# Optimization experiments

Measured on AMD Instinct MI355X. Metric: run time of the kernel, lower is better.

Reference implementation:

```python
import jax, jax.numpy as jnp
import numpy as np

N = 100000      # nodes
E = 1600000     # edges
IN_C = 64       # in_channels
HID = 128       # hidden_channels
K = 2           # Chebyshev order
EPS = 1e-5      # BatchNorm eps
SLOPE = 0.01    # LeakyReLU negative slope


def _glorot(key, shape, fan_in):
    lim = 1.0 / np.sqrt(fan_in)
    return jax.random.uniform(key, shape, jnp.float32, -lim, lim)


def setup_inputs() -> dict:
    key = jax.random.key(0)
    ks = jax.random.split(key, 12)
    x = jax.random.normal(ks[0], (N, IN_C), jnp.float32)
    edge_index = jax.random.randint(ks[1], (2, E), 0, N, dtype=jnp.int32)
    # ChebConv weights: one [Cin, Cout] matrix per Chebyshev order, plus bias.
    W1 = _glorot(ks[2], (K, IN_C, HID), IN_C)
    b1 = _glorot(ks[3], (HID,), IN_C)
    W2 = _glorot(ks[4], (K, HID, HID // 2), HID)
    b2 = _glorot(ks[5], (HID // 2,), HID)
    W3 = _glorot(ks[6], (K, HID // 2, IN_C), HID // 2)
    b3 = _glorot(ks[7], (IN_C,), HID // 2)
    # BatchNorm affine params
    gamma1 = jnp.ones((HID,), jnp.float32)
    beta1 = jnp.zeros((HID,), jnp.float32)
    gamma2 = jnp.ones((HID // 2,), jnp.float32)
    beta2 = jnp.zeros((HID // 2,), jnp.float32)
    return {"x": x, "edge_index": edge_index, "W1": W1, "b1": b1,
            "W2": W2, "b2": b2, "W3": W3, "b3": b3,
            "gamma1": gamma1, "beta1": beta1, "gamma2": gamma2, "beta2": beta2}


def reference(x, edge_index, W1, b1, W2, b2, W3, b3, gamma1, beta1, gamma2, beta2):
    row, col = edge_index[0], edge_index[1]
    # Scaled Laplacian with lambda_max=2 (PyG default): L_hat = -D^{-1/2} A D^{-1/2}
    deg = jax.ops.segment_sum(jnp.ones(row.shape, x.dtype), row, num_segments=N)
    dinv = jnp.where(deg > 0, jax.lax.rsqrt(jnp.where(deg > 0, deg, 1.0)), 0.0)
    ew = -dinv[row] * dinv[col]                     # [E] edge weights of L_hat

    def prop(h):  # y = L_hat @ h ; gather from source, scatter to target
        return jax.ops.segment_sum(ew[:, None] * h[row], col, num_segments=N)

    def cheb_conv(h, W, b):  # K=2: Tx0 = h, Tx1 = L_hat @ h
        return h @ W[0] + prop(h) @ W[1] + b

    def batchnorm(h, g, b):  # training-mode BN over node dim, biased variance
        m = h.mean(axis=0)
        v = jnp.mean(jnp.square(h - m), axis=0)
        return g * (h - m) * jax.lax.rsqrt(v + EPS) + b

    def lrelu(h):
        return jnp.where(h >= 0, h, SLOPE * h)

    h = lrelu(batchnorm(cheb_conv(x, W1, b1), gamma1, beta1))
    h = lrelu(batchnorm(cheb_conv(h, W2, b2), gamma2, beta2))
    return cheb_conv(h, W3, b3)
```

## Files before the change

kernel.cpp:

```cpp
#include <hip/hip_runtime.h>

#define NN 100000
#define NE 1600000
constexpr float BN_EPS = 1e-5f;
constexpr float LRELU_SLOPE = 0.01f;
constexpr int SC_NB = (NN + 255) / 256;
constexpr int RSH = 13;
constexpr int RB = 1 << RSH;
constexpr int NR = (NN + RB - 1) / RB;
constexpr int SB = 8;
constexpr int CAP = 163840;
constexpr int PBLK = 400;
constexpr int PCHUNK = NE / PBLK;

__global__ __launch_bounds__(256) void k_part(const int* __restrict__ row,
                                              const int* __restrict__ col,
                                              int* __restrict__ colCnt,
                                              int* __restrict__ rowCnt,
                                              int* __restrict__ colbuf,
                                              unsigned short* __restrict__ rowbuf) {
  __shared__ int cntc[NR], cntr[NR];
  const int tid = threadIdx.x;
  const int e0 = blockIdx.x * PCHUNK;
  if (tid < NR) { cntc[tid] = 0; cntr[tid] = 0; }
  __syncthreads();
  for (int i = tid; i < PCHUNK; i += 256) {
    atomicAdd(&cntc[col[e0 + i] >> RSH], 1);
    atomicAdd(&cntr[row[e0 + i] >> RSH], 1);
  }
  __syncthreads();
  if (tid < NR) {
    cntc[tid] = atomicAdd(&colCnt[tid], cntc[tid]);
  } else if (tid >= 64 && tid < 64 + NR) {
    const int b = tid - 64;
    cntr[b] = atomicAdd(&rowCnt[b], cntr[b]);
  }
  __syncthreads();
  for (int i = tid; i < PCHUNK; i += 256) {
    const int r = row[e0 + i];
    const int c = col[e0 + i];
    const int bc = c >> RSH;
    const int pc = atomicAdd(&cntc[bc], 1);
    colbuf[(size_t)bc * CAP + pc] = (r << RSH) | (c & (RB - 1));
    const int br = r >> RSH;
    const int pr = atomicAdd(&cntr[br], 1);
    rowbuf[(size_t)br * CAP + pr] = (unsigned short)(r & (RB - 1));
  }
}

__global__ __launch_bounds__(1024) void k_hist2(const int* __restrict__ colbuf,
                                                const unsigned short* __restrict__ rowbuf,
                                                const int* __restrict__ colCnt,
                                                const int* __restrict__ rowCnt,
                                                int* __restrict__ PDc,
                                                int* __restrict__ PDd) {
  __shared__ int h[RB];
  const int tid = threadIdx.x;
  const int b = blockIdx.x, s = blockIdx.y, z = blockIdx.z;
  for (int i = tid; i < RB; i += 1024) h[i] = 0;
  __syncthreads();
  const int len = z ? rowCnt[b] : colCnt[b];
  const int sl = (len + SB - 1) / SB;
  const int st = s * sl;
  const int en = min(st + sl, len);
  if (z == 0) {
    const int* cb = colbuf + (size_t)b * CAP;
    for (int i = st + tid; i < en; i += 1024)
      atomicAdd(&h[cb[i] & (RB - 1)], 1);
  } else {
    const unsigned short* rb = rowbuf + (size_t)b * CAP;
    for (int i = st + tid; i < en; i += 1024)
      atomicAdd(&h[rb[i]], 1);
  }
  __syncthreads();
  int* pd = (z ? PDd : PDc) + ((size_t)b * SB + s) * RB;
  for (int i = tid; i < RB; i += 1024) pd[i] = h[i];
}

__global__ __launch_bounds__(256) void k_csrmid2(const int* __restrict__ PDc,
                                                 const int* __restrict__ PDd,
                                                 int* __restrict__ Bpart,
                                                 int* __restrict__ cnt,
                                                 float* __restrict__ dinv) {
  const int n = blockIdx.x * 256 + threadIdx.x;
  if (n >= NN) return;
  const int b = n >> RSH, o = n & (RB - 1);
  int run = 0, dsum = 0;
#pragma unroll
  for (int s = 0; s < SB; s++) {
    Bpart[(size_t)s * NN + n] = run;
    run += PDc[((size_t)b * SB + s) * RB + o];
    dsum += PDd[((size_t)b * SB + s) * RB + o];
  }
  cnt[n] = run;
  dinv[n] = dsum > 0 ? rsqrtf((float)dsum) : 0.0f;
}

__global__ __launch_bounds__(256) void k_scan_a(const int* __restrict__ cnt,
                                                int* __restrict__ bsum) {
  __shared__ int sh[256];
  const int tid = threadIdx.x;
  const int i = blockIdx.x * 256 + tid;
  sh[tid] = (i < NN) ? cnt[i] : 0;
  __syncthreads();
  for (int st = 128; st > 0; st >>= 1) {
    if (tid < st) sh[tid] += sh[tid + st];
    __syncthreads();
  }
  if (tid == 0) bsum[blockIdx.x] = sh[0];
}

__global__ __launch_bounds__(512) void k_scan_b(const int* __restrict__ bsum,
                                                int* __restrict__ boff) {
  __shared__ int sh[512];
  const int tid = threadIdx.x;
  const int v = (tid < SC_NB) ? bsum[tid] : 0;
  sh[tid] = v;
  __syncthreads();
  for (int off = 1; off < 512; off <<= 1) {
    int t = (tid >= off) ? sh[tid - off] : 0;
    __syncthreads();
    sh[tid] += t;
    __syncthreads();
  }
  if (tid < SC_NB) boff[tid] = sh[tid] - v;
}

__global__ __launch_bounds__(256) void k_scan_c(const int* __restrict__ cnt,
                                                const int* __restrict__ boff,
                                                int* __restrict__ ptr) {
  __shared__ int sh[256];
  const int tid = threadIdx.x;
  const int i = blockIdx.x * 256 + tid;
  const int v = (i < NN) ? cnt[i] : 0;
  sh[tid] = v;
  __syncthreads();
  for (int off = 1; off < 256; off <<= 1) {
    int t = (tid >= off) ? sh[tid - off] : 0;
    __syncthreads();
    sh[tid] += t;
    __syncthreads();
  }
  const int excl = sh[tid] - v + boff[blockIdx.x];
  if (i < NN) {
    ptr[i] = excl;
    if (i == NN - 1) ptr[NN] = excl + v;
  }
}

__global__ __launch_bounds__(1024) void k_fill4(const int* __restrict__ colbuf,
                                                const int* __restrict__ colCnt,
                                                const int* __restrict__ ptr,
                                                const int* __restrict__ Bpart,
                                                int* __restrict__ eb) {
  __shared__ int cur[RB];
  const int tid = threadIdx.x;
  const int b = blockIdx.x, s = blockIdx.y;
  const int base = b << RSH;
  const int nmax = min(RB, NN - base);
  const int* bp = Bpart + (size_t)s * NN + base;
  for (int i = tid; i < nmax; i += 1024) cur[i] = ptr[base + i] + bp[i];
  __syncthreads();
  const int len = colCnt[b];
  const int sl = (len + SB - 1) / SB;
  const int st = s * sl;
  const int en = min(st + sl, len);
  const int* cb = colbuf + (size_t)b * CAP;
  for (int i = st + tid; i < en; i += 1024) {
    const int rec = cb[i];
    const int pos = atomicAdd(&cur[rec & (RB - 1)], 1);
    eb[pos] = rec >> RSH;
  }
}

__global__ __launch_bounds__(256) void k_scale(const float* __restrict__ x,
                                               const float* __restrict__ dinv,
                                               float* __restrict__ xs) {
  const size_t i = (size_t)blockIdx.x * 256 + threadIdx.x;
  const int n = (int)(i >> 4);
  float4 v = reinterpret_cast<const float4*>(x)[i];
  const float d = dinv[n];
  v.x *= d; v.y *= d; v.z *= d; v.w *= d;
  reinterpret_cast<float4*>(xs)[i] = v;
}

template <bool ADD>
__global__ __launch_bounds__(256) void k_prop64(const float* __restrict__ p,
                                                const int* __restrict__ eb,
                                                const int* __restrict__ ptr,
                                                const float* __restrict__ g,
                                                const float* __restrict__ dinv,
                                                float* __restrict__ out) {
  const int node = blockIdx.x * 16 + (threadIdx.x >> 4);
  const int lane = threadIdx.x & 15;
  if (node >= NN) return;
  const int b = ptr[node], e = ptr[node + 1];
  float4 a0 = make_float4(0.f, 0.f, 0.f, 0.f);
  float4 a1 = make_float4(0.f, 0.f, 0.f, 0.f);
  float4 a2 = make_float4(0.f, 0.f, 0.f, 0.f);
  float4 a3 = make_float4(0.f, 0.f, 0.f, 0.f);
  const float4* hp = reinterpret_cast<const float4*>(p) + lane;
  int j = b;
  for (; j + 4 <= e; j += 4) {
    const int s0 = eb[j], s1 = eb[j + 1], s2 = eb[j + 2], s3 = eb[j + 3];
    const float4 h0 = hp[(size_t)s0 * 16];
    const float4 h1 = hp[(size_t)s1 * 16];
    const float4 h2 = hp[(size_t)s2 * 16];
    const float4 h3 = hp[(size_t)s3 * 16];
    a0.x += h0.x; a0.y += h0.y; a0.z += h0.z; a0.w += h0.w;
    a1.x += h1.x; a1.y += h1.y; a1.z += h1.z; a1.w += h1.w;
    a2.x += h2.x; a2.y += h2.y; a2.z += h2.z; a2.w += h2.w;
    a3.x += h3.x; a3.y += h3.y; a3.z += h3.z; a3.w += h3.w;
  }
  for (; j + 2 <= e; j += 2) {
    const int s0 = eb[j], s1 = eb[j + 1];
    const float4 h0 = hp[(size_t)s0 * 16];
    const float4 h1 = hp[(size_t)s1 * 16];
    a0.x += h0.x; a0.y += h0.y; a0.z += h0.z; a0.w += h0.w;
    a1.x += h1.x; a1.y += h1.y; a1.z += h1.z; a1.w += h1.w;
  }
  if (j < e) {
    const float4 h0 = hp[(size_t)eb[j] * 16];
    a0.x += h0.x; a0.y += h0.y; a0.z += h0.z; a0.w += h0.w;
  }
  a0.x += a1.x + a2.x + a3.x;
  a0.y += a1.y + a2.y + a3.y;
  a0.z += a1.z + a2.z + a3.z;
  a0.w += a1.w + a2.w + a3.w;
  if (ADD) {
    const float dn = dinv[node];
    const float4 gv = reinterpret_cast<const float4*>(g)[(size_t)node * 16 + lane];
    a0.x = gv.x - dn * a0.x;
    a0.y = gv.y - dn * a0.y;
    a0.z = gv.z - dn * a0.z;
    a0.w = gv.w - dn * a0.w;
  }
  reinterpret_cast<float4*>(out)[(size_t)node * 16 + lane] = a0;
}

__global__ __launch_bounds__(512) void k_conv1(const float* __restrict__ x,
                                               const float* __restrict__ y,
                                               const float* __restrict__ dinv,
                                               const float* __restrict__ W,
                                               const float* __restrict__ bias,
                                               float* __restrict__ out) {
  __shared__ float XA[128][65];
  __shared__ float XY[128][65];
  const int tid = threadIdx.x;
  const int lane = tid & 63;
  const int wv = __builtin_amdgcn_readfirstlane(tid >> 6);
  const int n0 = blockIdx.x * 128;
  for (int idx = tid; idx < 2048; idx += 512) {
    const int n = idx >> 4, k4 = idx & 15;
    int node = n0 + n;
    if (node >= NN) node = NN - 1;
    const float4 av = *reinterpret_cast<const float4*>(x + (size_t)node * 64 + k4 * 4);
    float4 yv = *reinterpret_cast<const float4*>(y + (size_t)node * 64 + k4 * 4);
    const float dn = -dinv[node];
    yv.x *= dn; yv.y *= dn; yv.z *= dn; yv.w *= dn;
    float* da = &XA[n][k4 * 4];
    da[0] = av.x; da[1] = av.y; da[2] = av.z; da[3] = av.w;
    float* dy = &XY[n][k4 * 4];
    dy[0] = yv.x; dy[1] = yv.y; dy[2] = yv.z; dy[3] = yv.w;
  }
  __syncthreads();
  const int cw0 = wv * 16;
  const float* __restrict__ W0 = W + cw0;
  const float* __restrict__ W1 = W + 64 * 128 + cw0;
  float acc0[16], acc1[16];
#pragma unroll
  for (int j = 0; j < 16; j++) { acc0[j] = 0.f; acc1[j] = 0.f; }
#pragma unroll 2
  for (int k = 0; k < 64; k++) {
    const float a0 = XA[lane][k];
    const float a1 = XA[lane + 64][k];
    const float b0 = XY[lane][k];
    const float b1 = XY[lane + 64][k];
#pragma unroll
    for (int j = 0; j < 16; j++) {
      const float w0 = W0[(size_t)k * 128 + j];
      const float w1 = W1[(size_t)k * 128 + j];
      acc0[j] += a0 * w0 + b0 * w1;
      acc1[j] += a1 * w0 + b1 * w1;
    }
  }
#pragma unroll
  for (int half = 0; half < 2; half++) {
    const int node = n0 + lane + half * 64;
    const float* acc = half ? acc1 : acc0;
    if (node < NN) {
#pragma unroll
      for (int j = 0; j < 16; j += 4) {
        float4 o = make_float4(acc[j] + bias[cw0 + j], acc[j + 1] + bias[cw0 + j + 1],
                               acc[j + 2] + bias[cw0 + j + 2], acc[j + 3] + bias[cw0 + j + 3]);
        *reinterpret_cast<float4*>(out + (size_t)node * 128 + cw0 + j) = o;
      }
    }
  }
}

template <int Cin>
__global__ __launch_bounds__(512) void k_gemm_dual(const float* __restrict__ h,
                                                   const float* __restrict__ W,
                                                   const float* __restrict__ bias,
                                                   const float* __restrict__ scale,
                                                   const float* __restrict__ shift,
                                                   const float* __restrict__ dinv,
                                                   float* __restrict__ g,
                                                   float* __restrict__ p) {
  __shared__ float XA[128][Cin + 1];
  const int tid = threadIdx.x;
  const int lane = tid & 63;
  const int wv = __builtin_amdgcn_readfirstlane(tid >> 6);
  const int n0 = blockIdx.x * 128;
  constexpr int C4 = Cin / 4;
  for (int idx = tid; idx < 128 * C4; idx += 512) {
    const int n = idx / C4, k4 = idx % C4;
    int node = n0 + n;
    if (node >= NN) node = NN - 1;
    float4 v = *reinterpret_cast<const float4*>(h + (size_t)node * Cin + k4 * 4);
    const float4 sc = *reinterpret_cast<const float4*>(scale + k4 * 4);
    const float4 sh = *reinterpret_cast<const float4*>(shift + k4 * 4);
    v.x = sc.x * v.x + sh.x; v.y = sc.y * v.y + sh.y;
    v.z = sc.z * v.z + sh.z; v.w = sc.w * v.w + sh.w;
    v.x = v.x >= 0.f ? v.x : LRELU_SLOPE * v.x;
    v.y = v.y >= 0.f ? v.y : LRELU_SLOPE * v.y;
    v.z = v.z >= 0.f ? v.z : LRELU_SLOPE * v.z;
    v.w = v.w >= 0.f ? v.w : LRELU_SLOPE * v.w;
    float* d = &XA[n][k4 * 4];
    d[0] = v.x; d[1] = v.y; d[2] = v.z; d[3] = v.w;
  }
  __syncthreads();
  const int cw0 = wv * 8;
  const float* __restrict__ Wa = W + cw0;
  const float* __restrict__ Wb = W + Cin * 64 + cw0;
  float ag0[8], ag1[8], ap0[8], ap1[8];
#pragma unroll
  for (int j = 0; j < 8; j++) { ag0[j] = 0.f; ag1[j] = 0.f; ap0[j] = 0.f; ap1[j] = 0.f; }
#pragma unroll 2
  for (int k = 0; k < Cin; k++) {
    const float a0 = XA[lane][k];
    const float a1 = XA[lane + 64][k];
#pragma unroll
    for (int j = 0; j < 8; j++) {
      const float wa = Wa[(size_t)k * 64 + j];
      const float wb = Wb[(size_t)k * 64 + j];
      ag0[j] += a0 * wa; ag1[j] += a1 * wa;
      ap0[j] += a0 * wb; ap1[j] += a1 * wb;
    }
  }
#pragma unroll
  for (int half = 0; half < 2; half++) {
    const int node = n0 + lane + half * 64;
    const float* ag = half ? ag1 : ag0;
    const float* ap = half ? ap1 : ap0;
    if (node < NN) {
      const float dn = dinv[node];
#pragma unroll
      for (int j = 0; j < 8; j += 4) {
        float4 og = make_float4(ag[j] + bias[cw0 + j], ag[j + 1] + bias[cw0 + j + 1],
                                ag[j + 2] + bias[cw0 + j + 2], ag[j + 3] + bias[cw0 + j + 3]);
        *reinterpret_cast<float4*>(g + (size_t)node * 64 + cw0 + j) = og;
        float4 op = make_float4(ap[j] * dn, ap[j + 1] * dn, ap[j + 2] * dn, ap[j + 3] * dn);
        *reinterpret_cast<float4*>(p + (size_t)node * 64 + cw0 + j) = op;
      }
    }
  }
}

template <int C>
__global__ __launch_bounds__(256) void k_bnstats(const float* __restrict__ h,
                                                 float* __restrict__ bnsum,
                                                 float* __restrict__ bnsq) {
  constexpr int RPB = 256 / C;
  constexpr int ROWS = 256;
  const int c = threadIdx.x % C;
  const int g = threadIdx.x / C;
  const int r0 = blockIdx.x * ROWS + g;
  const int rend = min(blockIdx.x * ROWS + ROWS, NN);
  float s = 0.f, sq = 0.f;
  for (int r = r0; r < rend; r += RPB) {
    float v = h[(size_t)r * C + c];
    s += v;
    sq += v * v;
  }
  __shared__ float ss[256], sg[256];
  ss[threadIdx.x] = s;
  sg[threadIdx.x] = sq;
  __syncthreads();
  for (int st = 128; st >= C; st >>= 1) {
    if (threadIdx.x < st) {
      ss[threadIdx.x] += ss[threadIdx.x + st];
      sg[threadIdx.x] += sg[threadIdx.x + st];
    }
    __syncthreads();
  }
  if (threadIdx.x < C) {
    atomicAdd(&bnsum[threadIdx.x], ss[threadIdx.x]);
    atomicAdd(&bnsq[threadIdx.x], sg[threadIdx.x]);
  }
}

template <int C>
__global__ void k_bnfin(const float* __restrict__ bnsum, const float* __restrict__ bnsq,
                        const float* __restrict__ gamma, const float* __restrict__ beta,
                        float* __restrict__ scale, float* __restrict__ shift) {
  int c = threadIdx.x;
  if (c < C) {
    float mean = bnsum[c] * (1.0f / NN);
    float var = bnsq[c] * (1.0f / NN) - mean * mean;
    float sc = gamma[c] * rsqrtf(var + BN_EPS);
    scale[c] = sc;
    shift[c] = beta[c] - mean * sc;
  }
}

extern "C" void kernel_launch(void* const* d_in, const int* in_sizes, int n_in,
                              void* d_out, int out_size, void* d_ws, size_t ws_size,
                              hipStream_t stream) {
  const float* x   = (const float*)d_in[0];
  const int*   ei  = (const int*)d_in[1];
  const int*   row = ei;
  const int*   col = ei + NE;
  const float* W1  = (const float*)d_in[2];
  const float* b1  = (const float*)d_in[3];
  const float* W2  = (const float*)d_in[4];
  const float* b2  = (const float*)d_in[5];
  const float* W3  = (const float*)d_in[6];
  const float* b3  = (const float*)d_in[7];
  const float* g1  = (const float*)d_in[8];
  const float* be1 = (const float*)d_in[9];
  const float* g2w = (const float*)d_in[10];
  const float* be2 = (const float*)d_in[11];
  float* out = (float*)d_out;

  char* ws = (char*)d_ws;
  size_t off = 0;
  auto alloc = [&](size_t bytes) -> void* {
    void* p = ws + off;
    off = (off + bytes + 255) & ~(size_t)255;
    return p;
  };

  float* bnsum1 = (float*)alloc(128 * 4);
  float* bnsq1  = (float*)alloc(128 * 4);
  float* bnsum2 = (float*)alloc(64 * 4);
  float* bnsq2  = (float*)alloc(64 * 4);
  int*   colCnt = (int*)alloc(NR * 4);
  int*   rowCnt = (int*)alloc(NR * 4);
  const size_t zero_bytes = off;
  float* dinv   = (float*)alloc(NN * 4);
  int*   cnt    = (int*)alloc(NN * 4);
  int*   ptr    = (int*)alloc((NN + 1) * 4);
  int*   bsum   = (int*)alloc(SC_NB * 4);
  int*   boff   = (int*)alloc(SC_NB * 4);
  int*   eb     = (int*)alloc((size_t)NE * 4);
  float* scale1 = (float*)alloc(128 * 4);
  float* shift1 = (float*)alloc(128 * 4);
  float* scale2 = (float*)alloc(64 * 4);
  float* shift2 = (float*)alloc(64 * 4);
  float* bufA   = (float*)alloc((size_t)NN * 64 * 4);
  float* bufB   = (float*)alloc((size_t)NN * 128 * 4);
  float* bufC   = (float*)alloc((size_t)NN * 64 * 4);
  float* bufD   = (float*)alloc((size_t)NN * 64 * 4);

  int* colbuf = (int*)bufB;
  unsigned short* rowbuf = (unsigned short*)(colbuf + (size_t)NR * CAP);
  int* PDc    = (int*)bufC;
  int* PDd    = PDc + (size_t)NR * SB * RB;
  int* Bpart  = PDd + (size_t)NR * SB * RB;

  float* y1  = bufA;
  float* xs  = bufC;
  float* h1  = bufB;
  float* gg2 = bufA;
  float* p2  = bufC;
  float* h2  = bufD;
  float* gg3 = bufB;
  float* p3  = bufB + (size_t)NN * 64;

  hipMemsetAsync(d_ws, 0, zero_bytes, stream);

  k_part<<<PBLK, 256, 0, stream>>>(row, col, colCnt, rowCnt, colbuf, rowbuf);
  k_hist2<<<dim3(NR, SB, 2), 1024, 0, stream>>>(colbuf, rowbuf, colCnt, rowCnt, PDc, PDd);
  k_csrmid2<<<(NN + 255) / 256, 256, 0, stream>>>(PDc, PDd, Bpart, cnt, dinv);
  k_scan_a<<<SC_NB, 256, 0, stream>>>(cnt, bsum);
  k_scan_b<<<1, 512, 0, stream>>>(bsum, boff);
  k_scan_c<<<SC_NB, 256, 0, stream>>>(cnt, boff, ptr);
  k_fill4<<<dim3(NR, SB), 1024, 0, stream>>>(colbuf, colCnt, ptr, Bpart, eb);

  const int gemmGrid = (NN + 127) / 128;
  const int propGrid = (NN * 16 + 255) / 256;

  k_scale<<<NN * 16 / 256, 256, 0, stream>>>(x, dinv, xs);
  k_prop64<false><<<propGrid, 256, 0, stream>>>(xs, eb, ptr, nullptr, nullptr, y1);
  k_conv1<<<gemmGrid, 512, 0, stream>>>(x, y1, dinv, W1, b1, h1);
  k_bnstats<128><<<(NN + 255) / 256, 256, 0, stream>>>(h1, bnsum1, bnsq1);
  k_bnfin<128><<<1, 128, 0, stream>>>(bnsum1, bnsq1, g1, be1, scale1, shift1);

  k_gemm_dual<128><<<gemmGrid, 512, 0, stream>>>(h1, W2, b2, scale1, shift1, dinv, gg2, p2);
  k_prop64<true><<<propGrid, 256, 0, stream>>>(p2, eb, ptr, gg2, dinv, h2);
  k_bnstats<64><<<(NN + 255) / 256, 256, 0, stream>>>(h2, bnsum2, bnsq2);
  k_bnfin<64><<<1, 64, 0, stream>>>(bnsum2, bnsq2, g2w, be2, scale2, shift2);

  k_gemm_dual<64><<<gemmGrid, 512, 0, stream>>>(h2, W3, b3, scale2, shift2, dinv, gg3, p3);
  k_prop64<true><<<propGrid, 256, 0, stream>>>(p3, eb, ptr, gg3, dinv, out);
}
```

Measured before the change: 573.9 us.

## Fuse source scaling into first propagation and halve GEMM node tiles

Removes the separate k_scale pass by having the first propagation kernel multiply each gathered source row by dinv[src] on the fly, saving one full read/write of x. The conv1 and dual GEMM kernels now handle 64 nodes per block instead of 128, with padded shared rows and vectorised float2/float4 LDS reads and writes. This doubles the grid and lowers register pressure, but each weight load is reused across fewer nodes, and the fused propagation adds a scattered dinv load per edge.

```diff
diff --git a/kernel.cpp b/kernel.cpp
--- a/kernel.cpp
+++ b/kernel.cpp
@@ -173,18 +173,7 @@
   }
 }
 
-__global__ __launch_bounds__(256) void k_scale(const float* __restrict__ x,
-                                               const float* __restrict__ dinv,
-                                               float* __restrict__ xs) {
-  const size_t i = (size_t)blockIdx.x * 256 + threadIdx.x;
-  const int n = (int)(i >> 4);
-  float4 v = reinterpret_cast<const float4*>(x)[i];
-  const float d = dinv[n];
-  v.x *= d; v.y *= d; v.z *= d; v.w *= d;
-  reinterpret_cast<float4*>(xs)[i] = v;
-}
-
-template <bool ADD>
+template <bool SCALE, bool ADD>
 __global__ __launch_bounds__(256) void k_prop64(const float* __restrict__ p,
                                                 const int* __restrict__ eb,
                                                 const int* __restrict__ ptr,
@@ -203,25 +192,35 @@
   int j = b;
   for (; j + 4 <= e; j += 4) {
     const int s0 = eb[j], s1 = eb[j + 1], s2 = eb[j + 2], s3 = eb[j + 3];
+    const float w0 = SCALE ? dinv[s0] : 1.f;
+    const float w1 = SCALE ? dinv[s1] : 1.f;
+    const float w2 = SCALE ? dinv[s2] : 1.f;
+    const float w3 = SCALE ? dinv[s3] : 1.f;
     const float4 h0 = hp[(size_t)s0 * 16];
     const float4 h1 = hp[(size_t)s1 * 16];
     const float4 h2 = hp[(size_t)s2 * 16];
     const float4 h3 = hp[(size_t)s3 * 16];
-    a0.x += h0.x; a0.y += h0.y; a0.z += h0.z; a0.w += h0.w;
-    a1.x += h1.x; a1.y += h1.y; a1.z += h1.z; a1.w += h1.w;
-    a2.x += h2.x; a2.y += h2.y; a2.z += h2.z; a2.w += h2.w;
-    a3.x += h3.x; a3.y += h3.y; a3.z += h3.z; a3.w += h3.w;
-  }
-  for (; j + 2 <= e; j += 2) {
-    const int s0 = eb[j], s1 = eb[j + 1];
+    if (SCALE) {
+      a0.x += w0 * h0.x; a0.y += w0 * h0.y; a0.z += w0 * h0.z; a0.w += w0 * h0.w;
+      a1.x += w1 * h1.x; a1.y += w1 * h1.y; a1.z += w1 * h1.z; a1.w += w1 * h1.w;
+      a2.x += w2 * h2.x; a2.y += w2 * h2.y; a2.z += w2 * h2.z; a2.w += w2 * h2.w;
+      a3.x += w3 * h3.x; a3.y += w3 * h3.y; a3.z += w3 * h3.z; a3.w += w3 * h3.w;
+    } else {
+      a0.x += h0.x; a0.y += h0.y; a0.z += h0.z; a0.w += h0.w;
+      a1.x += h1.x; a1.y += h1.y; a1.z += h1.z; a1.w += h1.w;
+      a2.x += h2.x; a2.y += h2.y; a2.z += h2.z; a2.w += h2.w;
+      a3.x += h3.x; a3.y += h3.y; a3.z += h3.z; a3.w += h3.w;
+    }
+  }
+  for (; j < e; j++) {
+    const int s0 = eb[j];
+    const float w0 = SCALE ? dinv[s0] : 1.f;
     const float4 h0 = hp[(size_t)s0 * 16];
-    const float4 h1 = hp[(size_t)s1 * 16];
-    a0.x += h0.x; a0.y += h0.y; a0.z += h0.z; a0.w += h0.w;
-    a1.x += h1.x; a1.y += h1.y; a1.z += h1.z; a1.w += h1.w;
-  }
-  if (j < e) {
-    const float4 h0 = hp[(size_t)eb[j] * 16];
-    a0.x += h0.x; a0.y += h0.y; a0.z += h0.z; a0.w += h0.w;
+    if (SCALE) {
+      a0.x += w0 * h0.x; a0.y += w0 * h0.y; a0.z += w0 * h0.z; a0.w += w0 * h0.w;
+    } else {
+      a0.x += h0.x; a0.y += h0.y; a0.z += h0.z; a0.w += h0.w;
+    }
   }
   a0.x += a1.x + a2.x + a3.x;
   a0.y += a1.y + a2.y + a3.y;
@@ -244,13 +243,14 @@
                                                const float* __restrict__ W,
                                                const float* __restrict__ bias,
                                                float* __restrict__ out) {
-  __shared__ float XA[128][65];
-  __shared__ float XY[128][65];
+  constexpr int LDW = 68;
+  __shared__ float XA[64][LDW];
+  __shared__ float XY[64][LDW];
   const int tid = threadIdx.x;
   const int lane = tid & 63;
   const int wv = __builtin_amdgcn_readfirstlane(tid >> 6);
-  const int n0 = blockIdx.x * 128;
-  for (int idx = tid; idx < 2048; idx += 512) {
+  const int n0 = blockIdx.x * 64;
+  for (int idx = tid; idx < 1024; idx += 512) {
     const int n = idx >> 4, k4 = idx & 15;
     int node = n0 + n;
     if (node >= NN) node = NN - 1;
@@ -258,43 +258,35 @@
     float4 yv = *reinterpret_cast<const float4*>(y + (size_t)node * 64 + k4 * 4);
     const float dn = -dinv[node];
     yv.x *= dn; yv.y *= dn; yv.z *= dn; yv.w *= dn;
-    float* da = &XA[n][k4 * 4];
-    da[0] = av.x; da[1] = av.y; da[2] = av.z; da[3] = av.w;
-    float* dy = &XY[n][k4 * 4];
-    dy[0] = yv.x; dy[1] = yv.y; dy[2] = yv.z; dy[3] = yv.w;
+    *reinterpret_cast<float4*>(&XA[n][k4 * 4]) = av;
+    *reinterpret_cast<float4*>(&XY[n][k4 * 4]) = yv;
   }
   __syncthreads();
   const int cw0 = wv * 16;
   const float* __restrict__ W0 = W + cw0;
   const float* __restrict__ W1 = W + 64 * 128 + cw0;
-  float acc0[16], acc1[16];
-#pragma unroll
-  for (int j = 0; j < 16; j++) { acc0[j] = 0.f; acc1[j] = 0.f; }
+  float acc[16];
+#pragma unroll
+  for (int j = 0; j < 16; j++) acc[j] = 0.f;
 #pragma unroll 2
-  for (int k = 0; k < 64; k++) {
-    const float a0 = XA[lane][k];
-    const float a1 = XA[lane + 64][k];
-    const float b0 = XY[lane][k];
-    const float b1 = XY[lane + 64][k];
-#pragma unroll
-    for (int j = 0; j < 16; j++) {
-      const float w0 = W0[(size_t)k * 128 + j];
-      const float w1 = W1[(size_t)k * 128 + j];
-      acc0[j] += a0 * w0 + b0 * w1;
-      acc1[j] += a1 * w0 + b1 * w1;
-    }
-  }
-#pragma unroll
-  for (int half = 0; half < 2; half++) {
-    const int node = n0 + lane + half * 64;
-    const float* acc = half ? acc1 : acc0;
-    if (node < NN) {
-#pragma unroll
-      for (int j = 0; j < 16; j += 4) {
-        float4 o = make_float4(acc[j] + bias[cw0 + j], acc[j + 1] + bias[cw0 + j + 1],
-                               acc[j + 2] + bias[cw0 + j + 2], acc[j + 3] + bias[cw0 + j + 3]);
-        *reinterpret_cast<float4*>(out + (size_t)node * 128 + cw0 + j) = o;
-      }
+  for (int kc = 0; kc < 32; kc++) {
+    const float2 a2 = *reinterpret_cast<const float2*>(&XA[lane][kc * 2]);
+    const float2 y2 = *reinterpret_cast<const float2*>(&XY[lane][kc * 2]);
+    const int k0 = kc * 2;
+#pragma unroll
+    for (int j = 0; j < 16; j++)
+      acc[j] += a2.x * W0[(size_t)k0 * 128 + j] + y2.x * W1[(size_t)k0 * 128 + j];
+#pragma unroll
+    for (int j = 0; j < 16; j++)
+      acc[j] += a2.y * W0[(size_t)(k0 + 1) * 128 + j] + y2.y * W1[(size_t)(k0 + 1) * 128 + j];
+  }
+  const int node = n0 + lane;
+  if (node < NN) {
+#pragma unroll
+    for (int j = 0; j < 16; j += 4) {
+      float4 o = make_float4(acc[j] + bias[cw0 + j], acc[j + 1] + bias[cw0 + j + 1],
+                             acc[j + 2] + bias[cw0 + j + 2], acc[j + 3] + bias[cw0 + j + 3]);
+      *reinterpret_cast<float4*>(out + (size_t)node * 128 + cw0 + j) = o;
     }
   }
 }
@@ -308,13 +300,14 @@
                                                    const float* __restrict__ dinv,
                                                    float* __restrict__ g,
                                                    float* __restrict__ p) {
-  __shared__ float XA[128][Cin + 1];
+  constexpr int LDW = Cin + 4;
+  __shared__ float XA[64][LDW];
   const int tid = threadIdx.x;
   const int lane = tid & 63;
   const int wv = __builtin_amdgcn_readfirstlane(tid >> 6);
-  const int n0 = blockIdx.x * 128;
+  const int n0 = blockIdx.x * 64;
   constexpr int C4 = Cin / 4;
-  for (int idx = tid; idx < 128 * C4; idx += 512) {
+  for (int idx = tid; idx < 64 * C4; idx += 512) {
     const int n = idx / C4, k4 = idx % C4;
     int node = n0 + n;
     if (node >= NN) node = NN - 1;
@@ -327,43 +320,50 @@
     v.y = v.y >= 0.f ? v.y : LRELU_SLOPE * v.y;
     v.z = v.z >= 0.f ? v.z : LRELU_SLOPE * v.z;
     v.w = v.w >= 0.f ? v.w : LRELU_SLOPE * v.w;
-    float* d = &XA[n][k4 * 4];
-    d[0] = v.x; d[1] = v.y; d[2] = v.z; d[3] = v.w;
+    *reinterpret_cast<float4*>(&XA[n][k4 * 4]) = v;
   }
   __syncthreads();
   const int cw0 = wv * 8;
   const float* __restrict__ Wa = W + cw0;
   const float* __restrict__ Wb = W + Cin * 64 + cw0;
-  float ag0[8], ag1[8], ap0[8], ap1[8];
-#pragma unroll
-  for (int j = 0; j < 8; j++) { ag0[j] = 0.f; ag1[j] = 0.f; ap0[j] = 0.f; ap1[j] = 0.f; }
+  float ag[8], ap[8];
+#pragma unroll
+  for (int j = 0; j < 8; j++) { ag[j] = 0.f; ap[j] = 0.f; }
 #pragma unroll 2
-  for (int k = 0; k < Cin; k++) {
-    const float a0 = XA[lane][k];
-    const float a1 = XA[lane + 64][k];
+  for (int kc = 0; kc < C4; kc++) {
+    const float4 a4 = *reinterpret_cast<const float4*>(&XA[lane][kc * 4]);
+    const int k0 = kc * 4;
 #pragma unroll
     for (int j = 0; j < 8; j++) {
-      const float wa = Wa[(size_t)k * 64 + j];
-      const float wb = Wb[(size_t)k * 64 + j];
-      ag0[j] += a0 * wa; ag1[j] += a1 * wa;
-      ap0[j] += a0 * wb; ap1[j] += a1 * wb;
-    }
-  }
-#pragma unroll
-  for (int half = 0; half < 2; half++) {
-    const int node = n0 + lane + half * 64;
-    const float* ag = half ? ag1 : ag0;
-    const float* ap = half ? ap1 : ap0;
-    if (node < NN) {
-      const float dn = dinv[node];
-#pragma unroll
-      for (int j = 0; j < 8; j += 4) {
-        float4 og = make_float4(ag[j] + bias[cw0 + j], ag[j + 1] + bias[cw0 + j + 1],
-                                ag[j + 2] + bias[cw0 + j + 2], ag[j + 3] + bias[cw0 + j + 3]);
-        *reinterpret_cast<float4*>(g + (size_t)node * 64 + cw0 + j) = og;
-        float4 op = make_float4(ap[j] * dn, ap[j + 1] * dn, ap[j + 2] * dn, ap[j + 3] * dn);
-        *reinterpret_cast<float4*>(p + (size_t)node * 64 + cw0 + j) = op;
-      }
+      ag[j] += a4.x * Wa[(size_t)k0 * 64 + j];
+      ap[j] += a4.x * Wb[(size_t)k0 * 64 + j];
+    }
+#pragma unroll
+    for (int j = 0; j < 8; j++) {
+      ag[j] += a4.y * Wa[(size_t)(k0 + 1) * 64 + j];
+      ap[j] += a4.y * Wb[(size_t)(k0 + 1) * 64 + j];
+    }
+#pragma unroll
+    for (int j = 0; j < 8; j++) {
+      ag[j] += a4.z * Wa[(size_t)(k0 + 2) * 64 + j];
+      ap[j] += a4.z * Wb[(size_t)(k0 + 2) * 64 + j];
+    }
+#pragma unroll
+    for (int j = 0; j < 8; j++) {
+      ag[j] += a4.w * Wa[(size_t)(k0 + 3) * 64 + j];
+      ap[j] += a4.w * Wb[(size_t)(k0 + 3) * 64 + j];
+    }
+  }
+  const int node = n0 + lane;
+  if (node < NN) {
+    const float dn = dinv[node];
+#pragma unroll
+    for (int j = 0; j < 8; j += 4) {
+      float4 og = make_float4(ag[j] + bias[cw0 + j], ag[j + 1] + bias[cw0 + j + 1],
+                              ag[j + 2] + bias[cw0 + j + 2], ag[j + 3] + bias[cw0 + j + 3]);
+      *reinterpret_cast<float4*>(g + (size_t)node * 64 + cw0 + j) = og;
+      float4 op = make_float4(ap[j] * dn, ap[j + 1] * dn, ap[j + 2] * dn, ap[j + 3] * dn);
+      *reinterpret_cast<float4*>(p + (size_t)node * 64 + cw0 + j) = op;
     }
   }
 }
@@ -471,7 +471,6 @@
   int* Bpart  = PDd + (size_t)NR * SB * RB;
 
   float* y1  = bufA;
-  float* xs  = bufC;
   float* h1  = bufB;
   float* gg2 = bufA;
   float* p2  = bufC;
@@ -489,20 +488,19 @@
   k_scan_c<<<SC_NB, 256, 0, stream>>>(cnt, boff, ptr);
   k_fill4<<<dim3(NR, SB), 1024, 0, stream>>>(colbuf, colCnt, ptr, Bpart, eb);
 
-  const int gemmGrid = (NN + 127) / 128;
+  const int gemmGrid = (NN + 63) / 64;
   const int propGrid = (NN * 16 + 255) / 256;
 
-  k_scale<<<NN * 16 / 256, 256, 0, stream>>>(x, dinv, xs);
-  k_prop64<false><<<propGrid, 256, 0, stream>>>(xs, eb, ptr, nullptr, nullptr, y1);
+  k_prop64<true, false><<<propGrid, 256, 0, stream>>>(x, eb, ptr, nullptr, dinv, y1);
   k_conv1<<<gemmGrid, 512, 0, stream>>>(x, y1, dinv, W1, b1, h1);
   k_bnstats<128><<<(NN + 255) / 256, 256, 0, stream>>>(h1, bnsum1, bnsq1);
   k_bnfin<128><<<1, 128, 0, stream>>>(bnsum1, bnsq1, g1, be1, scale1, shift1);
 
   k_gemm_dual<128><<<gemmGrid, 512, 0, stream>>>(h1, W2, b2, scale1, shift1, dinv, gg2, p2);
-  k_prop64<true><<<propGrid, 256, 0, stream>>>(p2, eb, ptr, gg2, dinv, h2);
+  k_prop64<false, true><<<propGrid, 256, 0, stream>>>(p2, eb, ptr, gg2, dinv, h2);
   k_bnstats<64><<<(NN + 255) / 256, 256, 0, stream>>>(h2, bnsum2, bnsq2);
   k_bnfin<64><<<1, 64, 0, stream>>>(bnsum2, bnsq2, g2w, be2, scale2, shift2);
 
   k_gemm_dual<64><<<gemmGrid, 512, 0, stream>>>(h2, W3, b3, scale2, shift2, dinv, gg3, p3);
-  k_prop64<true><<<propGrid, 256, 0, stream>>>(p3, eb, ptr, gg3, dinv, out);
-}
+  k_prop64<false, true><<<propGrid, 256, 0, stream>>>(p3, eb, ptr, gg3, dinv, out);
+}
```

Measured after the change: 566.0 us. Within noise of the previous version (-1.4%).
